# Optimization experiments

Hardware: AMD Instinct MI355X
Metric: run time of the kernel (lower is better)

Reference implementation:

```python
import jax, jax.numpy as jnp
import numpy as np

HIDDEN = 1024
OUT = 8192
N_SUBJ = 8
B = 64
T = 512


def setup_inputs() -> dict:
    key = jax.random.key(0)
    ks = jax.random.split(key, 12)
    s = 1.0 / np.sqrt(HIDDEN)
    return {
        "context": jax.random.normal(ks[0], (B, T, HIDDEN), dtype=jnp.float32),
        "subject_ids": jax.random.randint(ks[1], (B,), 0, N_SUBJ),
        "eps": jax.random.normal(ks[2], (B, OUT), dtype=jnp.float32),
        # pool_proj: Linear(H,H) -> GELU -> Linear(H,H); weights stored (in,out)
        "w1": jax.random.normal(ks[3], (HIDDEN, HIDDEN), dtype=jnp.float32) * s,
        "b1": jax.random.normal(ks[4], (HIDDEN,), dtype=jnp.float32) * s,
        "w2": jax.random.normal(ks[5], (HIDDEN, HIDDEN), dtype=jnp.float32) * s,
        "b2": jax.random.normal(ks[6], (HIDDEN,), dtype=jnp.float32) * s,
        # SubjectLayers params, init normal(0, 1/sqrt(in))
        "subj_w": jax.random.normal(ks[7], (N_SUBJ, HIDDEN, OUT), dtype=jnp.float32) * s,
        "subj_b": jax.random.normal(ks[8], (N_SUBJ, OUT), dtype=jnp.float32) * s,
        # log_var head: weight std 1e-4, bias -2.0
        "lv_w": jax.random.normal(ks[9], (HIDDEN, OUT), dtype=jnp.float32) * 1e-4,
        "lv_b": jnp.full((OUT,), -2.0, dtype=jnp.float32),
    }


def reference(context, subject_ids, eps, w1, b1, w2, b2, subj_w, subj_b, lv_w, lv_b):
    # mean-pool over time: (B,T,H) -> (B,H)
    h = context.mean(axis=1)
    # pool_proj MLP with exact GELU (torch default)
    h = jax.nn.gelu(h @ w1 + b1, approximate=False) @ w2 + b2
    # per-subject linear head: gather (H,OUT) weight per sample, matvec
    w = subj_w[subject_ids]            # (B, H, OUT)
    mu = jnp.einsum("bd,bdo->bo", h, w) + subj_b[subject_ids]
    # variational log-variance head, clamped
    log_var = jnp.clip(h @ lv_w + lv_b, -10.0, 2.0)
    # reparameterized sample (training mode)
    x0 = mu + eps * jnp.exp(0.5 * log_var)
    return x0, mu, log_var
```

## Files before the change

kernel.cpp:

```cpp
#include <hip/hip_runtime.h>
#include <math.h>

#define HID   1024
#define OUTD  8192
#define NSUBJ 8
#define BATCH 64
#define TLEN  512

#define OFF_PP    0u
#define OFF_P1    1048576u
#define OFF_P2    3145728u
#define OFF_H     5242880u
#define OFF_MUP   5308416u
#define OFF_LVP   9502720u

__global__ __launch_bounds__(256) void k_pool(const float* __restrict__ ctx,
                                              float* __restrict__ pp) {
    int b  = blockIdx.x;
    int tc = blockIdx.y;
    int hid = threadIdx.x * 4;
    const float* base = ctx + ((size_t)b * TLEN + (size_t)tc * 32) * HID + hid;
    float4 acc = make_float4(0.f, 0.f, 0.f, 0.f);
#pragma unroll 8
    for (int t = 0; t < 32; ++t) {
        float4 v = *(const float4*)(base + (size_t)t * HID);
        acc.x += v.x; acc.y += v.y; acc.z += v.z; acc.w += v.w;
    }
    *(float4*)(pp + ((size_t)tc * BATCH + b) * HID + hid) = acc;
}

__global__ __launch_bounds__(256) void k_mlp1(const float* __restrict__ pp,
                                              const float* __restrict__ w1,
                                              float* __restrict__ p1) {
    __shared__ float xs[32][34];
    int j  = blockIdx.x * 256 + threadIdx.x;
    int k0 = blockIdx.y * 32;
    int b0 = blockIdx.z * 32;
    {
        int bb = threadIdx.x >> 3;
        int kk = (threadIdx.x & 7) * 4;
        float4 s = make_float4(0.f, 0.f, 0.f, 0.f);
#pragma unroll
        for (int tc = 0; tc < 16; ++tc) {
            float4 v = *(const float4*)(pp + (size_t)tc * 65536 + (b0 + bb) * 1024 + k0 + kk);
            s.x += v.x; s.y += v.y; s.z += v.z; s.w += v.w;
        }
        const float inv = 1.0f / 512.0f;
        xs[bb][kk]     = s.x * inv;
        xs[bb][kk + 1] = s.y * inv;
        xs[bb][kk + 2] = s.z * inv;
        xs[bb][kk + 3] = s.w * inv;
    }
    __syncthreads();
    float acc[32];
#pragma unroll
    for (int i = 0; i < 32; ++i) acc[i] = 0.f;
    for (int kk = 0; kk < 32; kk += 2) {
        float wa = w1[(size_t)(k0 + kk) * HID + j];
        float wb = w1[(size_t)(k0 + kk + 1) * HID + j];
#pragma unroll
        for (int i = 0; i < 32; ++i) {
            acc[i] = fmaf(xs[i][kk], wa, acc[i]);
            acc[i] = fmaf(xs[i][kk + 1], wb, acc[i]);
        }
    }
    float* dst = p1 + (size_t)blockIdx.y * 65536;
#pragma unroll
    for (int i = 0; i < 32; ++i) dst[(b0 + i) * 1024 + j] = acc[i];
}

__global__ __launch_bounds__(256) void k_mlp2(const float* __restrict__ p1,
                                              const float* __restrict__ b1,
                                              const float* __restrict__ w2,
                                              float* __restrict__ p2) {
    __shared__ float xs[32][34];
    int j  = blockIdx.x * 256 + threadIdx.x;
    int k0 = blockIdx.y * 32;
    int b0 = blockIdx.z * 32;
    {
        int bb = threadIdx.x >> 3;
        int kk = (threadIdx.x & 7) * 4;
        float4 s = make_float4(0.f, 0.f, 0.f, 0.f);
#pragma unroll
        for (int kc = 0; kc < 32; ++kc) {
            float4 v = *(const float4*)(p1 + (size_t)kc * 65536 + (b0 + bb) * 1024 + k0 + kk);
            s.x += v.x; s.y += v.y; s.z += v.z; s.w += v.w;
        }
        float4 bbv = *(const float4*)(b1 + k0 + kk);
        s.x += bbv.x; s.y += bbv.y; s.z += bbv.z; s.w += bbv.w;
        const float r = 0.70710678118654752f;
        xs[bb][kk]     = 0.5f * s.x * (1.0f + erff(s.x * r));
        xs[bb][kk + 1] = 0.5f * s.y * (1.0f + erff(s.y * r));
        xs[bb][kk + 2] = 0.5f * s.z * (1.0f + erff(s.z * r));
        xs[bb][kk + 3] = 0.5f * s.w * (1.0f + erff(s.w * r));
    }
    __syncthreads();
    float acc[32];
#pragma unroll
    for (int i = 0; i < 32; ++i) acc[i] = 0.f;
    for (int kk = 0; kk < 32; kk += 2) {
        float wa = w2[(size_t)(k0 + kk) * HID + j];
        float wb = w2[(size_t)(k0 + kk + 1) * HID + j];
#pragma unroll
        for (int i = 0; i < 32; ++i) {
            acc[i] = fmaf(xs[i][kk], wa, acc[i]);
            acc[i] = fmaf(xs[i][kk + 1], wb, acc[i]);
        }
    }
    float* dst = p2 + (size_t)blockIdx.y * 65536;
#pragma unroll
    for (int i = 0; i < 32; ++i) dst[(b0 + i) * 1024 + j] = acc[i];
}

__global__ __launch_bounds__(256) void k_red_bias(const float* __restrict__ p,
                                                  const float* __restrict__ bias,
                                                  float* __restrict__ out) {
    int i = (blockIdx.x * 256 + threadIdx.x) * 4;
    int j = i & (HID - 1);
    float4 s = make_float4(0.f, 0.f, 0.f, 0.f);
#pragma unroll
    for (int kc = 0; kc < 32; ++kc) {
        float4 v = *(const float4*)(p + (size_t)kc * 65536 + i);
        s.x += v.x; s.y += v.y; s.z += v.z; s.w += v.w;
    }
    float4 bb = *(const float4*)(bias + j);
    s.x += bb.x; s.y += bb.y; s.z += bb.z; s.w += bb.w;
    *(float4*)(out + i) = s;
}

template <int NS>
__device__ __forceinline__ void mu_tile(const float* __restrict__ hmat,
                                        const float* __restrict__ wbase,
                                        float* __restrict__ mup_kc,
                                        const int* bo, int n, int k0, int o) {
    float4 acc[NS];
#pragma unroll
    for (int i = 0; i < NS; ++i) acc[i] = make_float4(0.f, 0.f, 0.f, 0.f);
    float4 wv[4];
#pragma unroll
    for (int kk = 0; kk < 4; ++kk)
        wv[kk] = *(const float4*)(wbase + (size_t)(k0 + kk) * OUTD + o);
    for (int k = k0; k < k0 + 128; k += 4) {
        float4 hv[NS];
#pragma unroll
        for (int i = 0; i < NS; ++i)
            hv[i] = *(const float4*)(hmat + bo[i] * HID + k);
        int kn = (k + 4 < k0 + 128) ? (k + 4) : k0;
        float4 wn[4];
#pragma unroll
        for (int kk = 0; kk < 4; ++kk)
            wn[kk] = *(const float4*)(wbase + (size_t)(kn + kk) * OUTD + o);
#pragma unroll
        for (int kk = 0; kk < 4; ++kk) {
            float4 w = wv[kk];
#pragma unroll
            for (int i = 0; i < NS; ++i) {
                float h = (kk == 0) ? hv[i].x : (kk == 1) ? hv[i].y
                        : (kk == 2) ? hv[i].z : hv[i].w;
                acc[i].x = fmaf(h, w.x, acc[i].x);
                acc[i].y = fmaf(h, w.y, acc[i].y);
                acc[i].z = fmaf(h, w.z, acc[i].z);
                acc[i].w = fmaf(h, w.w, acc[i].w);
            }
        }
#pragma unroll
        for (int kk = 0; kk < 4; ++kk) wv[kk] = wn[kk];
    }
#pragma unroll
    for (int i = 0; i < NS; ++i)
        if (i < n) *(float4*)(mup_kc + (size_t)bo[i] * OUTD + o) = acc[i];
}

__global__ __launch_bounds__(256) void k_mu(const float* __restrict__ hmat,
                                            const float* __restrict__ subj_w,
                                            const int* __restrict__ sid,
                                            float* __restrict__ mup) {
    int o  = blockIdx.x * 1024 + threadIdx.x * 4;
    int k0 = blockIdx.y * 128;
    int s  = blockIdx.z;
    int lane = threadIdx.x & 63;
    int mysid = sid[lane];
    unsigned long long m = __ballot(mysid == s);
    int ns = __popcll(m);
    if (ns == 0) return;
    const float* wbase = subj_w + (size_t)s * HID * OUTD;
    float* mup_kc = mup + (size_t)blockIdx.y * BATCH * OUTD;
    unsigned long long mm = m;
    for (int base = 0; base < ns; base += 12) {
        int take = ns - base; if (take > 12) take = 12;
        int fb = (int)__builtin_ctzll(mm);
        int bo[12];
#pragma unroll
        for (int i = 0; i < 12; ++i) {
            bo[i] = (mm != 0ull) ? (int)__builtin_ctzll(mm) : fb;
            if (mm != 0ull) mm &= (mm - 1ull);
        }
        if (take <= 4)       mu_tile<4>(hmat, wbase, mup_kc, bo, take, k0, o);
        else if (take <= 8)  mu_tile<8>(hmat, wbase, mup_kc, bo, take, k0, o);
        else                 mu_tile<12>(hmat, wbase, mup_kc, bo, take, k0, o);
    }
}

__global__ __launch_bounds__(256) void k_lv(const float* __restrict__ hmat,
                                            const float* __restrict__ lv_w,
                                            float* __restrict__ lvp) {
    int o  = blockIdx.x * 512 + threadIdx.x * 2;
    int k0 = blockIdx.y * 128;
    int b0 = blockIdx.z * 32;
    float2 acc[32];
#pragma unroll
    for (int i = 0; i < 32; ++i) acc[i] = make_float2(0.f, 0.f);
    float2 wv0 = *(const float2*)(lv_w + (size_t)k0 * OUTD + o);
    float2 wv1 = *(const float2*)(lv_w + (size_t)(k0 + 1) * OUTD + o);
    for (int k = k0; k < k0 + 128; k += 2) {
        float2 hv[32];
#pragma unroll
        for (int i = 0; i < 32; ++i)
            hv[i] = *(const float2*)(hmat + (b0 + i) * HID + k);
        int kn = (k + 2 < k0 + 128) ? (k + 2) : k0;
        float2 wn0 = *(const float2*)(lv_w + (size_t)kn * OUTD + o);
        float2 wn1 = *(const float2*)(lv_w + (size_t)(kn + 1) * OUTD + o);
#pragma unroll
        for (int i = 0; i < 32; ++i) {
            acc[i].x = fmaf(hv[i].x, wv0.x, acc[i].x);
            acc[i].y = fmaf(hv[i].x, wv0.y, acc[i].y);
            acc[i].x = fmaf(hv[i].y, wv1.x, acc[i].x);
            acc[i].y = fmaf(hv[i].y, wv1.y, acc[i].y);
        }
        wv0 = wn0; wv1 = wn1;
    }
#pragma unroll
    for (int i = 0; i < 32; ++i) {
        float* dst = lvp + ((size_t)blockIdx.y * BATCH + b0 + i) * OUTD + o;
        dst[0] = acc[i].x; dst[1] = acc[i].y;
    }
}

__global__ __launch_bounds__(256) void k_combine(const float* __restrict__ mup,
                                                 const float* __restrict__ lvp,
                                                 const float* __restrict__ eps,
                                                 const float* __restrict__ subj_b,
                                                 const float* __restrict__ lv_b,
                                                 const int* __restrict__ sid,
                                                 float* __restrict__ out) {
    int idx = (blockIdx.x * 256 + threadIdx.x) * 4;
    int b = idx >> 13;
    int o = idx & (OUTD - 1);
    float4 m = make_float4(0.f, 0.f, 0.f, 0.f);
    float4 l = make_float4(0.f, 0.f, 0.f, 0.f);
#pragma unroll
    for (int kc = 0; kc < 8; ++kc) {
        float4 t = *(const float4*)(mup + (size_t)kc * 524288 + idx);
        m.x += t.x; m.y += t.y; m.z += t.z; m.w += t.w;
        float4 u = *(const float4*)(lvp + (size_t)kc * 524288 + idx);
        l.x += u.x; l.y += u.y; l.z += u.z; l.w += u.w;
    }
    int s = sid[b];
    float4 sb = *(const float4*)(subj_b + s * OUTD + o);
    float4 lb = *(const float4*)(lv_b + o);
    m.x += sb.x; m.y += sb.y; m.z += sb.z; m.w += sb.w;
    l.x = fminf(fmaxf(l.x + lb.x, -10.f), 2.f);
    l.y = fminf(fmaxf(l.y + lb.y, -10.f), 2.f);
    l.z = fminf(fmaxf(l.z + lb.z, -10.f), 2.f);
    l.w = fminf(fmaxf(l.w + lb.w, -10.f), 2.f);
    float4 e = *(const float4*)(eps + idx);
    float4 x0;
    x0.x = m.x + e.x * __expf(0.5f * l.x);
    x0.y = m.y + e.y * __expf(0.5f * l.y);
    x0.z = m.z + e.z * __expf(0.5f * l.z);
    x0.w = m.w + e.w * __expf(0.5f * l.w);
    *(float4*)(out + idx) = x0;
    *(float4*)(out + 524288 + idx) = m;
    *(float4*)(out + 1048576 + idx) = l;
}

extern "C" void kernel_launch(void* const* d_in, const int* in_sizes, int n_in,
                              void* d_out, int out_size, void* d_ws, size_t ws_size,
                              hipStream_t stream) {
    const float* ctx    = (const float*)d_in[0];
    const int*   sid    = (const int*)  d_in[1];
    const float* eps    = (const float*)d_in[2];
    const float* w1     = (const float*)d_in[3];
    const float* b1     = (const float*)d_in[4];
    const float* w2     = (const float*)d_in[5];
    const float* b2     = (const float*)d_in[6];
    const float* subj_w = (const float*)d_in[7];
    const float* subj_b = (const float*)d_in[8];
    const float* lv_w   = (const float*)d_in[9];
    const float* lv_b   = (const float*)d_in[10];
    float* out = (float*)d_out;

    float* ws   = (float*)d_ws;
    float* pp   = ws + OFF_PP;
    float* p1   = ws + OFF_P1;
    float* p2   = ws + OFF_P2;
    float* hbuf = ws + OFF_H;
    float* mup  = ws + OFF_MUP;
    float* lvp  = ws + OFF_LVP;

    k_pool<<<dim3(BATCH, 16), 256, 0, stream>>>(ctx, pp);
    k_mlp1<<<dim3(4, 32, 2), 256, 0, stream>>>(pp, w1, p1);
    k_mlp2<<<dim3(4, 32, 2), 256, 0, stream>>>(p1, b1, w2, p2);
    k_red_bias<<<64, 256, 0, stream>>>(p2, b2, hbuf);
    k_mu<<<dim3(8, 8, NSUBJ), 256, 0, stream>>>(hbuf, subj_w, sid, mup);
    k_lv<<<dim3(16, 8, 2), 256, 0, stream>>>(hbuf, lv_w, lvp);
    k_combine<<<512, 256, 0, stream>>>(mup, lvp, eps, subj_b, lv_b, sid, out);
}
```

Baseline: 184.6 us.

## Fuse subject-mu and log-var heads into one launch with finer lv K-split

Replaces the separate k_mu and k_lv kernels with a single k_head launch. Its first 512 blocks run the per-subject mu tiles and the remaining 512 blocks compute log-var using the shared mu_tile routine, now templated on K length. The lv work is split into 16 K-chunks of 64 with 16 batch rows per wavefront, and k_combine sums the 16 lv partials. The aim is to remove a launch gap, let lv blocks fill CUs left idle by exited mu blocks, and raise lv parallelism. In exchange, lv partial-sum traffic doubles and the workspace must hold twice as many lv partials.

Result: faster. 176.0 us (-4.7%).

```diff
diff --git a/kernel.cpp b/kernel.cpp
--- a/kernel.cpp
+++ b/kernel.cpp
@@ -128,10 +128,10 @@
     *(float4*)(out + i) = s;
 }
 
-template <int NS>
+template <int NS, int KLEN>
 __device__ __forceinline__ void mu_tile(const float* __restrict__ hmat,
                                         const float* __restrict__ wbase,
-                                        float* __restrict__ mup_kc,
+                                        float* __restrict__ dst_kc,
                                         const int* bo, int n, int k0, int o) {
     float4 acc[NS];
 #pragma unroll
@@ -140,12 +140,12 @@
 #pragma unroll
     for (int kk = 0; kk < 4; ++kk)
         wv[kk] = *(const float4*)(wbase + (size_t)(k0 + kk) * OUTD + o);
-    for (int k = k0; k < k0 + 128; k += 4) {
+    for (int k = k0; k < k0 + KLEN; k += 4) {
         float4 hv[NS];
 #pragma unroll
         for (int i = 0; i < NS; ++i)
             hv[i] = *(const float4*)(hmat + bo[i] * HID + k);
-        int kn = (k + 4 < k0 + 128) ? (k + 4) : k0;
+        int kn = (k + 4 < k0 + KLEN) ? (k + 4) : k0;
         float4 wn[4];
 #pragma unroll
         for (int kk = 0; kk < 4; ++kk)
@@ -168,71 +168,54 @@
     }
 #pragma unroll
     for (int i = 0; i < NS; ++i)
-        if (i < n) *(float4*)(mup_kc + (size_t)bo[i] * OUTD + o) = acc[i];
-}
-
-__global__ __launch_bounds__(256) void k_mu(const float* __restrict__ hmat,
-                                            const float* __restrict__ subj_w,
-                                            const int* __restrict__ sid,
-                                            float* __restrict__ mup) {
-    int o  = blockIdx.x * 1024 + threadIdx.x * 4;
-    int k0 = blockIdx.y * 128;
-    int s  = blockIdx.z;
-    int lane = threadIdx.x & 63;
-    int mysid = sid[lane];
-    unsigned long long m = __ballot(mysid == s);
-    int ns = __popcll(m);
-    if (ns == 0) return;
-    const float* wbase = subj_w + (size_t)s * HID * OUTD;
-    float* mup_kc = mup + (size_t)blockIdx.y * BATCH * OUTD;
-    unsigned long long mm = m;
-    for (int base = 0; base < ns; base += 12) {
-        int take = ns - base; if (take > 12) take = 12;
-        int fb = (int)__builtin_ctzll(mm);
-        int bo[12];
-#pragma unroll
-        for (int i = 0; i < 12; ++i) {
-            bo[i] = (mm != 0ull) ? (int)__builtin_ctzll(mm) : fb;
-            if (mm != 0ull) mm &= (mm - 1ull);
-        }
-        if (take <= 4)       mu_tile<4>(hmat, wbase, mup_kc, bo, take, k0, o);
-        else if (take <= 8)  mu_tile<8>(hmat, wbase, mup_kc, bo, take, k0, o);
-        else                 mu_tile<12>(hmat, wbase, mup_kc, bo, take, k0, o);
-    }
-}
-
-__global__ __launch_bounds__(256) void k_lv(const float* __restrict__ hmat,
-                                            const float* __restrict__ lv_w,
-                                            float* __restrict__ lvp) {
-    int o  = blockIdx.x * 512 + threadIdx.x * 2;
-    int k0 = blockIdx.y * 128;
-    int b0 = blockIdx.z * 32;
-    float2 acc[32];
-#pragma unroll
-    for (int i = 0; i < 32; ++i) acc[i] = make_float2(0.f, 0.f);
-    float2 wv0 = *(const float2*)(lv_w + (size_t)k0 * OUTD + o);
-    float2 wv1 = *(const float2*)(lv_w + (size_t)(k0 + 1) * OUTD + o);
-    for (int k = k0; k < k0 + 128; k += 2) {
-        float2 hv[32];
-#pragma unroll
-        for (int i = 0; i < 32; ++i)
-            hv[i] = *(const float2*)(hmat + (b0 + i) * HID + k);
-        int kn = (k + 2 < k0 + 128) ? (k + 2) : k0;
-        float2 wn0 = *(const float2*)(lv_w + (size_t)kn * OUTD + o);
-        float2 wn1 = *(const float2*)(lv_w + (size_t)(kn + 1) * OUTD + o);
-#pragma unroll
-        for (int i = 0; i < 32; ++i) {
-            acc[i].x = fmaf(hv[i].x, wv0.x, acc[i].x);
-            acc[i].y = fmaf(hv[i].x, wv0.y, acc[i].y);
-            acc[i].x = fmaf(hv[i].y, wv1.x, acc[i].x);
-            acc[i].y = fmaf(hv[i].y, wv1.y, acc[i].y);
-        }
-        wv0 = wn0; wv1 = wn1;
-    }
-#pragma unroll
-    for (int i = 0; i < 32; ++i) {
-        float* dst = lvp + ((size_t)blockIdx.y * BATCH + b0 + i) * OUTD + o;
-        dst[0] = acc[i].x; dst[1] = acc[i].y;
+        if (i < n) *(float4*)(dst_kc + (size_t)bo[i] * OUTD + o) = acc[i];
+}
+
+__global__ __launch_bounds__(256) void k_head(const float* __restrict__ hbuf,
+                                              const float* __restrict__ subj_w,
+                                              const float* __restrict__ lv_w,
+                                              const int* __restrict__ sid,
+                                              float* __restrict__ mup,
+                                              float* __restrict__ lvp) {
+    int blk = blockIdx.x;
+    int tid = threadIdx.x;
+    if (blk < 512) {
+        int o  = (blk & 7) * 1024 + tid * 4;
+        int k0 = ((blk >> 3) & 7) * 128;
+        int s  = blk >> 6;
+        int lane = tid & 63;
+        int mysid = sid[lane];
+        unsigned long long m = __ballot(mysid == s);
+        int ns = __popcll(m);
+        if (ns == 0) return;
+        const float* wbase = subj_w + (size_t)s * HID * OUTD;
+        float* mup_kc = mup + (size_t)((blk >> 3) & 7) * BATCH * OUTD;
+        unsigned long long mm = m;
+        for (int base = 0; base < ns; base += 12) {
+            int take = ns - base; if (take > 12) take = 12;
+            int fb = (int)__builtin_ctzll(mm);
+            int bo[12];
+#pragma unroll
+            for (int i = 0; i < 12; ++i) {
+                bo[i] = (mm != 0ull) ? (int)__builtin_ctzll(mm) : fb;
+                if (mm != 0ull) mm &= (mm - 1ull);
+            }
+            if (take <= 4)       mu_tile<4, 128>(hbuf, wbase, mup_kc, bo, take, k0, o);
+            else if (take <= 8)  mu_tile<8, 128>(hbuf, wbase, mup_kc, bo, take, k0, o);
+            else                 mu_tile<12, 128>(hbuf, wbase, mup_kc, bo, take, k0, o);
+        }
+    } else {
+        int u   = blk - 512;
+        int wid = tid >> 6;
+        int lane = tid & 63;
+        int o  = (u & 31) * 256 + lane * 4;
+        int k0 = (u >> 5) * 64;
+        int s0 = wid * 16;
+        int bo[16];
+#pragma unroll
+        for (int i = 0; i < 16; ++i) bo[i] = s0 + i;
+        float* lvp_kc = lvp + (size_t)(u >> 5) * BATCH * OUTD;
+        mu_tile<16, 64>(hbuf, lv_w, lvp_kc, bo, 16, k0, o);
     }
 }
 
@@ -252,6 +235,9 @@
     for (int kc = 0; kc < 8; ++kc) {
         float4 t = *(const float4*)(mup + (size_t)kc * 524288 + idx);
         m.x += t.x; m.y += t.y; m.z += t.z; m.w += t.w;
+    }
+#pragma unroll
+    for (int kc = 0; kc < 16; ++kc) {
         float4 u = *(const float4*)(lvp + (size_t)kc * 524288 + idx);
         l.x += u.x; l.y += u.y; l.z += u.z; l.w += u.w;
     }
@@ -302,7 +288,6 @@
     k_mlp1<<<dim3(4, 32, 2), 256, 0, stream>>>(pp, w1, p1);
     k_mlp2<<<dim3(4, 32, 2), 256, 0, stream>>>(p1, b1, w2, p2);
     k_red_bias<<<64, 256, 0, stream>>>(p2, b2, hbuf);
-    k_mu<<<dim3(8, 8, NSUBJ), 256, 0, stream>>>(hbuf, subj_w, sid, mup);
-    k_lv<<<dim3(16, 8, 2), 256, 0, stream>>>(hbuf, lv_w, lvp);
+    k_head<<<1024, 256, 0, stream>>>(hbuf, subj_w, lv_w, sid, mup, lvp);
     k_combine<<<512, 256, 0, stream>>>(mup, lvp, eps, subj_b, lv_b, sid, out);
 }
```
